# Kernel tuning notes

Hardware: AMD Instinct MI355X
Metric: run time of the kernel (lower is better)

## Reference

```python
import jax, jax.numpy as jnp
import numpy as np

N_HEAD = 16
TEMPERATURE = 1.0
LORA_SCALING = 16.0 / 8.0  # lora_alpha / r


def setup_inputs() -> dict:
    key = jax.random.key(0)
    B, S, D, E, R = 4, 1024, 1024, 8, 8
    ks = jax.random.split(key, 24)
    it = iter(ks)

    def nrm(shape, s):
        return (jax.random.normal(next(it), shape, jnp.float32) * s)

    inp = {}
    inp['x'] = jax.random.normal(next(it), (B, S, D), jnp.float32)
    inp['conv_w'] = nrm((D, D, 3), 0.02)
    inp['conv_b'] = jnp.zeros((D,), jnp.float32)
    inp['pool_w'] = nrm((1, D), 0.02)
    inp['pool_b'] = jnp.zeros((1,), jnp.float32)
    inp['rlin_w'] = nrm((E, D), 0.02)
    inp['rlin_b'] = jnp.zeros((E,), jnp.float32)
    for p, has_bias in (('q', True), ('k', False), ('v', True), ('o', True)):
        inp[p + 'W'] = nrm((D, D), 0.02)
        if has_bias:
            inp[p + 'b'] = jnp.zeros((D,), jnp.float32)
        inp[p + 'A'] = nrm((E, R, D), 0.02)
        inp[p + 'B'] = nrm((E, D, R), 0.02)
    return inp


def _router(x, conv_w, conv_b, pool_w, pool_b, rlin_w, rlin_b):
    # Conv1d(kernel=3, padding=1) over sequence, channels = n_state
    xc = jax.lax.conv_general_dilated(
        x.transpose(0, 2, 1), conv_w, (1,), [(1, 1)],
        dimension_numbers=('NCH', 'OIH', 'NCH')) + conv_b[None, :, None]
    xp = xc.transpose(0, 2, 1)                      # [B, S, D]
    scores = xp @ pool_w.T + pool_b                 # [B, S, 1]
    w = jax.nn.softmax(scores, axis=1)
    pooled = jnp.sum(w * xp, axis=1)                # [B, D]
    logits = pooled @ rlin_w.T + rlin_b             # [B, E]
    return jax.nn.softmax(logits / TEMPERATURE, axis=-1)


def _moe_linear(x, W, b, A, Bm, route):
    base = x @ W.T
    if b is not None:
        base = base + b
    h = jnp.einsum('bsd,erd->besr', x, A)           # [B, E, S, r]
    lora = jnp.einsum('besr,enr,be->bsn', h, Bm, route)
    return base + LORA_SCALING * lora


def reference(x, conv_w, conv_b, pool_w, pool_b, rlin_w, rlin_b,
              qW, qb, qA, qB, kW, kA, kB, vW, vb, vA, vB, oW, ob, oA, oB):
    B, S, D = x.shape
    H = N_HEAD
    dh = D // H
    route = _router(x, conv_w, conv_b, pool_w, pool_b, rlin_w, rlin_b)

    q = _moe_linear(x, qW, qb, qA, qB, route)
    k = _moe_linear(x, kW, None, kA, kB, route)
    v = _moe_linear(x, vW, vb, vA, vB, route)

    scale = dh ** (-0.25)
    qh = q.reshape(B, S, H, dh).transpose(0, 2, 1, 3) * scale   # [B,H,S,dh]
    kh = k.reshape(B, S, H, dh).transpose(0, 2, 3, 1) * scale   # [B,H,dh,S]
    vh = v.reshape(B, S, H, dh).transpose(0, 2, 1, 3)           # [B,H,S,dh]

    qk = (qh @ kh).astype(jnp.float32)                          # [B,H,S,S]
    w = jax.nn.softmax(qk, axis=-1).astype(q.dtype)
    wv = (w @ vh).transpose(0, 2, 1, 3).reshape(B, S, D)

    out = _moe_linear(wv, oW, ob, oA, oB, route)
    return out, qk
```

## Files before the change

kernel.cpp:

```cpp
#include <hip/hip_runtime.h>
#include <cstdint>

typedef unsigned short u16;
typedef __bf16 bf16_t;
typedef bf16_t bf16x8 __attribute__((ext_vector_type(8)));
typedef float f32x4 __attribute__((ext_vector_type(4)));

#define B_ 4
#define S_ 1024
#define D_ 1024
#define E_ 8
#define R_ 8
#define H_ 16
#define DH_ 64

#define GLOAD16(gp, lp) __builtin_amdgcn_global_load_lds( \
        (const __attribute__((address_space(1))) void*)(gp), \
        (__attribute__((address_space(3))) void*)(lp), 16, 0, 0)

static __device__ __forceinline__ u16 f2b(float f){
    union { float f; uint32_t i; } v; v.f = f;
    uint32_t i = v.i;
    uint32_t r = i + 0x7FFFu + ((i >> 16) & 1u);
    return (u16)(r >> 16);
}

__global__ void k_cvtall(const float4* x, const float* qB, const float* kB,
                         const float* vB, const float* oB,
                         ushort4* x16, ushort4* B16v, float4* cwp4){
    const int NX = B_*S_*D_/4;
    const int NB = E_*D_*R_/4;
    const int NC = 3*D_/4;
    const int NTOT = NX + 4*NB + NC;
    for (int i = blockIdx.x*blockDim.x + threadIdx.x; i < NTOT; i += gridDim.x*blockDim.x){
        if (i < NX){
            float4 v = x[i];
            ushort4 o; o.x=f2b(v.x); o.y=f2b(v.y); o.z=f2b(v.z); o.w=f2b(v.w);
            x16[i] = o;
        } else if (i < NX + 4*NB){
            int j = i - NX;
            int p = j >> 14, e = j & (NB-1);
            const float4* src = (p==0)?(const float4*)qB:(p==1)?(const float4*)kB
                              :(p==2)?(const float4*)vB:(const float4*)oB;
            float4 v = src[e];
            ushort4 o; o.x=f2b(v.x); o.y=f2b(v.y); o.z=f2b(v.z); o.w=f2b(v.w);
            B16v[p*NB + e] = o;
        } else {
            cwp4[i - NX - 4*NB] = make_float4(0.f,0.f,0.f,0.f);
        }
    }
}

__global__ void k_cwp(const float* conv_w, const float* conv_b, const float* pool_w,
                      const float* pool_b, float* cwp, float* constk){
    __shared__ float red[256];
    int bid = blockIdx.x, ob = blockIdx.y;
    if (bid < 12){
        int j = bid*256 + threadIdx.x;
        int t = j >> 10, i = j & 1023;
        float acc = 0.f;
        for (int o = ob*128; o < (ob+1)*128; ++o)
            acc += pool_w[o] * conv_w[(size_t)o*3072 + i*3 + t];
        atomicAdd(&cwp[j], acc);
    } else if (ob == 0){
        float acc = 0.f;
        for (int o = threadIdx.x; o < D_; o += 256) acc += pool_w[o] * conv_b[o];
        red[threadIdx.x] = acc; __syncthreads();
        for (int s = 128; s > 0; s >>= 1){
            if (threadIdx.x < s) red[threadIdx.x] += red[threadIdx.x+s];
            __syncthreads();
        }
        if (threadIdx.x == 0) *constk = red[0] + pool_b[0];
    }
}

__global__ void k_h(const float* x, const float* cwp, float* h){
    int b = blockIdx.y;
    int w = threadIdx.x >> 6, lane = threadIdx.x & 63;
    int s = blockIdx.x*4 + w;
    const float4* xr = (const float4*)(x + ((size_t)b*S_ + s)*D_);
    const float4* c0 = (const float4*)(cwp);
    const float4* c1 = (const float4*)(cwp + D_);
    const float4* c2 = (const float4*)(cwp + 2*D_);
    float a0 = 0.f, a1 = 0.f, a2 = 0.f;
    #pragma unroll
    for (int it = 0; it < 4; ++it){
        float4 v  = xr[it*64 + lane];
        float4 w0 = c0[it*64 + lane];
        float4 w1 = c1[it*64 + lane];
        float4 w2 = c2[it*64 + lane];
        a0 += v.x*w0.x + v.y*w0.y + v.z*w0.z + v.w*w0.w;
        a1 += v.x*w1.x + v.y*w1.y + v.z*w1.z + v.w*w1.w;
        a2 += v.x*w2.x + v.y*w2.y + v.z*w2.z + v.w*w2.w;
    }
    for (int off = 32; off; off >>= 1){
        a0 += __shfl_down(a0, off);
        a1 += __shfl_down(a1, off);
        a2 += __shfl_down(a2, off);
    }
    if (lane == 0){
        h[(0*B_ + b)*S_ + s] = a0;
        h[(1*B_ + b)*S_ + s] = a1;
        h[(2*B_ + b)*S_ + s] = a2;
    }
}

__global__ void k_xw(const float* x, const float* h, const float* constk, float* xwl){
    int b = blockIdx.y;
    int lane = threadIdx.x & 63;
    int w = threadIdx.x >> 6;
    int i = blockIdx.x*64 + lane;
    __shared__ float red[256];
    __shared__ float wsm_l[S_];
    __shared__ float red3[3][4][64];
    const float* h0 = h + (0*B_ + b)*S_;
    const float* h1 = h + (1*B_ + b)*S_;
    const float* h2 = h + (2*B_ + b)*S_;
    float ck = *constk;
    float mx = -1e30f;
    for (int s = threadIdx.x; s < S_; s += 256){
        float v = h1[s] + ck;
        if (s >= 1)   v += h0[s-1];
        if (s+1 < S_) v += h2[s+1];
        wsm_l[s] = v;
        mx = fmaxf(mx, v);
    }
    red[threadIdx.x] = mx; __syncthreads();
    for (int st = 128; st > 0; st >>= 1){
        if (threadIdx.x < st) red[threadIdx.x] = fmaxf(red[threadIdx.x], red[threadIdx.x+st]);
        __syncthreads();
    }
    mx = red[0]; __syncthreads();
    float sum = 0.f;
    for (int s = threadIdx.x; s < S_; s += 256) sum += __expf(wsm_l[s] - mx);
    red[threadIdx.x] = sum; __syncthreads();
    for (int st = 128; st > 0; st >>= 1){
        if (threadIdx.x < st) red[threadIdx.x] += red[threadIdx.x+st];
        __syncthreads();
    }
    float inv = 1.f / red[0];
    __syncthreads();
    for (int s = threadIdx.x; s < S_; s += 256)
        wsm_l[s] = __expf(wsm_l[s] - mx) * inv;
    __syncthreads();
    const float* xb = x + (size_t)b*S_*D_;
    float a0 = 0.f, a1 = 0.f, a2 = 0.f;
    #pragma unroll 4
    for (int r = w*256; r < (w+1)*256; ++r){
        float xv = xb[(size_t)r*D_ + i];
        float w1 = wsm_l[r];
        float w0 = (r+1 < S_) ? wsm_l[r+1] : 0.f;
        float w2 = (r >= 1)   ? wsm_l[r-1] : 0.f;
        a0 += w0*xv; a1 += w1*xv; a2 += w2*xv;
    }
    red3[0][w][lane] = a0; red3[1][w][lane] = a1; red3[2][w][lane] = a2;
    __syncthreads();
    if (w == 0){
        a0 = red3[0][0][lane] + red3[0][1][lane] + red3[0][2][lane] + red3[0][3][lane];
        a1 = red3[1][0][lane] + red3[1][1][lane] + red3[1][2][lane] + red3[1][3][lane];
        a2 = red3[2][0][lane] + red3[2][1][lane] + red3[2][2][lane] + red3[2][3][lane];
        xwl[b*3072 + i*3 + 0] = a0;
        xwl[b*3072 + i*3 + 1] = a1;
        xwl[b*3072 + i*3 + 2] = a2;
    }
}

__global__ void k_pooled(const float* conv_w, const float* conv_b, const float* xwl, float* pooled){
    int o = blockIdx.x*4 + (threadIdx.x >> 6);
    int lane = threadIdx.x & 63;
    const float* cw = conv_w + (size_t)o*3072;
    float a0=0.f, a1=0.f, a2=0.f, a3=0.f;
    for (int j = lane; j < 3072; j += 64){
        float c = cw[j];
        a0 += c*xwl[j]; a1 += c*xwl[3072+j]; a2 += c*xwl[2*3072+j]; a3 += c*xwl[3*3072+j];
    }
    for (int off = 32; off; off >>= 1){
        a0 += __shfl_down(a0, off); a1 += __shfl_down(a1, off);
        a2 += __shfl_down(a2, off); a3 += __shfl_down(a3, off);
    }
    if (lane == 0){
        float cb = conv_b[o];
        pooled[0*D_+o] = a0+cb; pooled[1*D_+o] = a1+cb;
        pooled[2*D_+o] = a2+cb; pooled[3*D_+o] = a3+cb;
    }
}

__global__ void k_route(const float* pooled, const float* rlin_w, const float* rlin_b, float* route){
    __shared__ float lg[B_][E_];
    int t = threadIdx.x;
    int b = t >> 6, e = (t >> 3) & 7, part = t & 7;
    float acc = 0.f;
    for (int o = part; o < D_; o += 8) acc += pooled[b*D_+o] * rlin_w[e*D_+o];
    acc += __shfl_down(acc, 4); acc += __shfl_down(acc, 2); acc += __shfl_down(acc, 1);
    if (part == 0) lg[b][e] = acc + rlin_b[e];
    __syncthreads();
    if (t < B_){
        float mx = -1e30f;
        for (int e2 = 0; e2 < E_; ++e2) mx = fmaxf(mx, lg[t][e2]);
        float ex[E_], sum = 0.f;
        for (int e2 = 0; e2 < E_; ++e2){ ex[e2] = expf(lg[t][e2]-mx); sum += ex[e2]; }
        for (int e2 = 0; e2 < E_; ++e2) route[t*E_+e2] = ex[e2]/sum;
    }
}

__global__ void k_aeff(const float* qA, const float* kA, const float* vA, const float* oA,
                       const float* route, u16* AeffT){
    int dc = blockIdx.x, b = blockIdx.y, p = blockIdx.z;
    const float* Ap = (p==0)?qA:(p==1)?kA:(p==2)?vA:oA;
    int z = p*4 + b;
    for (int idx = threadIdx.x; idx < 64*64; idx += 256){
        int dl = idx >> 6, kk = idx & 63;
        int d = dc*64 + dl;
        int e = kk >> 3, r = kk & 7;
        float v = 2.0f * route[b*E_+e] * Ap[(size_t)(e*R_+r)*D_ + d];
        AeffT[((size_t)z*D_ + d)*64 + kk] = f2b(v);
    }
}

__global__ __launch_bounds__(256) void k_weff(
        const u16* B16,
        const float* qW, const float* kW, const float* vW, const float* oW,
        const u16* AeffT, u16* Weff){
    __shared__ __align__(16) u16 As[128*64];
    __shared__ __align__(16) u16 Bs[128*64];
    int z = blockIdx.z, p = z >> 2;
    const u16* Bp = B16 + (size_t)p*E_*D_*R_;
    const float* Wp = (p==0)?qW:(p==1)?kW:(p==2)?vW:oW;
    int n0 = blockIdx.x*128, d0 = blockIdx.y*128;
    int tid = threadIdx.x;
    int e = tid & 7, row = tid >> 3;
    for (int pass = 0; pass < 4; ++pass){
        int rr = row + pass*32;
        GLOAD16(&Bp[((size_t)e*D_ + (n0+rr))*R_],           &As[pass*2048 + tid*8]);
        GLOAD16(&AeffT[((size_t)z*D_ + (d0+rr))*64 + e*8],  &Bs[pass*2048 + tid*8]);
    }
    __syncthreads();
    int l = tid & 63, w = tid >> 6;
    int wm = (w & 1)*64, wn = (w >> 1)*64;
    int lr = l & 15, quad = l >> 4;
    f32x4 acc[4][4] = {};
    for (int kk = 0; kk < 64; kk += 32){
        bf16x8 af[4], bg[4];
        for (int i = 0; i < 4; ++i) af[i] = *(const bf16x8*)&As[(wm + i*16 + lr)*64 + kk + quad*8];
        for (int j = 0; j < 4; ++j) bg[j] = *(const bf16x8*)&Bs[(wn + j*16 + lr)*64 + kk + quad*8];
        for (int i = 0; i < 4; ++i)
            for (int j = 0; j < 4; ++j)
                acc[i][j] = __builtin_amdgcn_mfma_f32_16x16x32_bf16(af[i], bg[j], acc[i][j], 0, 0, 0);
    }
    u16* Wz = Weff + (size_t)z*D_*D_;
    for (int i = 0; i < 4; ++i)
        for (int j = 0; j < 4; ++j)
            for (int r2 = 0; r2 < 4; ++r2){
                int n = n0 + wm + i*16 + quad*4 + r2;
                int d = d0 + wn + j*16 + lr;
                Wz[(size_t)n*D_ + d] = f2b(acc[i][j][r2] + Wp[(size_t)n*D_ + d]);
            }
}

static __device__ __forceinline__ void gemm_body(
        const u16* __restrict__ A, int lda,
        const u16* __restrict__ Bw,
        u16* Cb, float* Cf, int ldc,
        const float* bias, float scale, int K,
        int m0, int n0)
{
    __shared__ __align__(16) u16 As[128*32];
    __shared__ __align__(16) u16 Bs[128*32];
    int tid = threadIdx.x;
    int srow = tid >> 2, skc = (tid & 3)*8;
    u16* asd = &As[tid*8];
    u16* bsd = &Bs[tid*8];
    const u16* ga0 = &A [(size_t)(m0+srow)*lda + skc];
    const u16* ga1 = &A [(size_t)(m0+srow+64)*lda + skc];
    const u16* gb0 = &Bw[(size_t)(n0+srow)*D_ + skc];
    const u16* gb1 = &Bw[(size_t)(n0+srow+64)*D_ + skc];
    int l = tid & 63, w = tid >> 6;
    int wm = (w & 1)*64, wn = (w >> 1)*64;
    int lr = l & 15, quad = l >> 4;
    f32x4 acc[4][4] = {};
    for (int k0 = 0; k0 < K; k0 += 32){
        __syncthreads();
        GLOAD16(ga0 + k0, asd);
        GLOAD16(ga1 + k0, asd + 2048);
        GLOAD16(gb0 + k0, bsd);
        GLOAD16(gb1 + k0, bsd + 2048);
        __syncthreads();
        bf16x8 af[4], bg[4];
        for (int i = 0; i < 4; ++i) af[i] = *(const bf16x8*)&As[(wm + i*16 + lr)*32 + quad*8];
        for (int j = 0; j < 4; ++j) bg[j] = *(const bf16x8*)&Bs[(wn + j*16 + lr)*32 + quad*8];
        for (int i = 0; i < 4; ++i)
            for (int j = 0; j < 4; ++j)
                acc[i][j] = __builtin_amdgcn_mfma_f32_16x16x32_bf16(af[i], bg[j], acc[i][j], 0, 0, 0);
    }
    for (int j = 0; j < 4; ++j){
        int n = n0 + wn + j*16 + lr;
        float bv = bias ? bias[n] : 0.f;
        for (int i = 0; i < 4; ++i){
            int mrow = m0 + wm + i*16 + quad*4;
            for (int r2 = 0; r2 < 4; ++r2){
                float val = (acc[i][j][r2] + bv) * scale;
                size_t idx = (size_t)(mrow+r2)*ldc + n;
                if (Cf) __builtin_nontemporal_store(val, &Cf[idx]);
                else    Cb[idx] = f2b(val);
            }
        }
    }
}

__global__ __launch_bounds__(256) void k_gemm_qkv(
        const u16* x16, const u16* Weff, u16* qkv, const float* qb, const float* vb){
    int z = blockIdx.z, p = z >> 2, b = z & 3;
    const float* bias = (p==0) ? qb : (p==2) ? vb : (const float*)nullptr;
    float scale = (p==2) ? 1.0f : 0.35355339059327373f;
    gemm_body(x16 + (size_t)b*S_*D_, D_,
              Weff + (size_t)z*D_*D_,
              qkv + (size_t)z*S_*D_, (float*)nullptr, D_,
              bias, scale, 1024, blockIdx.x*128, blockIdx.y*128);
}

__global__ __launch_bounds__(256) void k_gemm_o(
        const u16* wv, const u16* WeffO, float* out, const float* ob){
    int b = blockIdx.z;
    gemm_body(wv + (size_t)b*S_*D_, D_,
              WeffO + (size_t)b*D_*D_,
              (u16*)nullptr, out + (size_t)b*S_*D_, D_,
              ob, 1.0f, 1024, blockIdx.x*128, blockIdx.y*128);
}

__global__ void k_vtrans(const u16* v, u16* vT){
    __shared__ __align__(16) u16 Tl[64*72];
    int st = blockIdx.x, bh = blockIdx.y;
    int b = bh >> 4, h = bh & 15;
    int tid = threadIdx.x;
    int row = tid >> 3, c = (tid & 7)*8;
    const u16* vb = v + (size_t)b*S_*D_ + h*64;
    for (int pass = 0; pass < 2; ++pass){
        int r = row + pass*32;
        *(uint4*)&Tl[r*72 + c] = *(const uint4*)&vb[(size_t)(st*64 + r)*D_ + c];
    }
    __syncthreads();
    u16* vTb = vT + (size_t)bh*64*S_;
    for (int pass = 0; pass < 2; ++pass){
        int dr = row + pass*32;
        union { u16 s[8]; uint4 u; } tmp;
        for (int j = 0; j < 8; ++j) tmp.s[j] = Tl[(c+j)*72 + dr];
        *(uint4*)&vTb[(size_t)dr*S_ + st*64 + c] = tmp.u;
    }
}

__global__ __launch_bounds__(256) void k_attn(const u16* q, const u16* k, const u16* vT,
                                              float* qk_out, u16* wv){
    __shared__ __align__(16) u16 Ql[64*64];
    __shared__ __align__(16) u16 Kl[64*64];
    __shared__ __align__(16) u16 Vt[64*64];
    __shared__ __align__(16) u16 Pl[64*64];
    int qt = blockIdx.x, bh = blockIdx.y;
    int b = bh >> 4, h = bh & 15;
    int q0 = qt*64;
    int tid = threadIdx.x;
    int l = tid & 63, w = tid >> 6;
    int lr = l & 15, quad = l >> 4;
    int srow = tid >> 3;
    int scol = (((tid & 7) ^ ((tid >> 3) & 7))) * 8;
    int sdst = tid * 8;
    const u16* qp  = q  + (size_t)b*S_*D_ + h*64;
    const u16* kp  = k  + (size_t)b*S_*D_ + h*64;
    const u16* vTp = vT + (size_t)bh*64*S_;
    float* qko = qk_out + (size_t)bh*S_*S_;
    GLOAD16(&qp[(size_t)(q0 + srow)*D_ + scol],      &Ql[sdst]);
    GLOAD16(&qp[(size_t)(q0 + srow + 32)*D_ + scol], &Ql[sdst + 2048]);
    int rsw = lr & 7;
    f32x4 oacc[4] = {};
    float m_i[4], l_i[4];
    for (int r2 = 0; r2 < 4; ++r2){ m_i[r2] = -1e30f; l_i[r2] = 0.f; }
    for (int t0 = 0; t0 < S_; t0 += 64){
        __syncthreads();
        GLOAD16(&kp[(size_t)(t0 + srow)*D_ + scol],        &Kl[sdst]);
        GLOAD16(&kp[(size_t)(t0 + srow + 32)*D_ + scol],   &Kl[sdst + 2048]);
        GLOAD16(&vTp[(size_t)srow*S_ + t0 + scol],         &Vt[sdst]);
        GLOAD16(&vTp[(size_t)(srow + 32)*S_ + t0 + scol],  &Vt[sdst + 2048]);
        __syncthreads();
        f32x4 sacc[4] = {};
        for (int kk = 0; kk < 64; kk += 32){
            int un = ((quad + (kk >> 3)) ^ rsw) * 8;
            bf16x8 aq = *(const bf16x8*)&Ql[(w*16 + lr)*64 + un];
            for (int jn = 0; jn < 4; ++jn){
                bf16x8 bk = *(const bf16x8*)&Kl[(jn*16 + lr)*64 + un];
                sacc[jn] = __builtin_amdgcn_mfma_f32_16x16x32_bf16(aq, bk, sacc[jn], 0, 0, 0);
            }
        }
        for (int jn = 0; jn < 4; ++jn)
            for (int r2 = 0; r2 < 4; ++r2){
                int sq = q0 + w*16 + quad*4 + r2;
                __builtin_nontemporal_store(sacc[jn][r2], &qko[(size_t)sq*S_ + t0 + jn*16 + lr]);
            }
        float alpha[4];
        for (int r2 = 0; r2 < 4; ++r2){
            float mx = fmaxf(fmaxf(sacc[0][r2], sacc[1][r2]), fmaxf(sacc[2][r2], sacc[3][r2]));
            for (int off = 1; off < 16; off <<= 1) mx = fmaxf(mx, __shfl_xor(mx, off));
            float mnew = fmaxf(m_i[r2], mx);
            alpha[r2] = __expf(m_i[r2] - mnew);
            m_i[r2] = mnew;
        }
        f32x4 p[4];
        for (int jn = 0; jn < 4; ++jn)
            for (int r2 = 0; r2 < 4; ++r2)
                p[jn][r2] = __expf(sacc[jn][r2] - m_i[r2]);
        for (int r2 = 0; r2 < 4; ++r2){
            float s = p[0][r2] + p[1][r2] + p[2][r2] + p[3][r2];
            for (int off = 1; off < 16; off <<= 1) s += __shfl_xor(s, off);
            l_i[r2] = l_i[r2]*alpha[r2] + s;
        }
        for (int jn = 0; jn < 4; ++jn)
            for (int r2 = 0; r2 < 4; ++r2)
                oacc[jn][r2] *= alpha[r2];
        for (int jn = 0; jn < 4; ++jn)
            for (int r2 = 0; r2 < 4; ++r2){
                int pr = w*16 + quad*4 + r2;
                int tu = (jn*2 + (lr >> 3)) ^ (pr & 7);
                Pl[pr*64 + tu*8 + (lr & 7)] = f2b(p[jn][r2]);
            }
        for (int kk = 0; kk < 64; kk += 32){
            int un = ((quad + (kk >> 3)) ^ rsw) * 8;
            bf16x8 ap = *(const bf16x8*)&Pl[(w*16 + lr)*64 + un];
            for (int jn = 0; jn < 4; ++jn){
                bf16x8 bv = *(const bf16x8*)&Vt[(jn*16 + lr)*64 + un];
                oacc[jn] = __builtin_amdgcn_mfma_f32_16x16x32_bf16(ap, bv, oacc[jn], 0, 0, 0);
            }
        }
    }
    u16* wvp = wv + (size_t)b*S_*D_ + h*64;
    for (int r2 = 0; r2 < 4; ++r2){
        float inv = 1.f / l_i[r2];
        int sq = q0 + w*16 + quad*4 + r2;
        for (int jn = 0; jn < 4; ++jn)
            wvp[(size_t)sq*D_ + jn*16 + lr] = f2b(oacc[jn][r2] * inv);
    }
}

extern "C" void kernel_launch(void* const* d_in, const int* in_sizes, int n_in,
                              void* d_out, int out_size, void* d_ws, size_t ws_size,
                              hipStream_t stream){
    const float* x      = (const float*)d_in[0];
    const float* conv_w = (const float*)d_in[1];
    const float* conv_b = (const float*)d_in[2];
    const float* pool_w = (const float*)d_in[3];
    const float* pool_b = (const float*)d_in[4];
    const float* rlin_w = (const float*)d_in[5];
    const float* rlin_b = (const float*)d_in[6];
    const float* qW = (const float*)d_in[7];
    const float* qb = (const float*)d_in[8];
    const float* qA = (const float*)d_in[9];
    const float* qB = (const float*)d_in[10];
    const float* kW = (const float*)d_in[11];
    const float* kA = (const float*)d_in[12];
    const float* kB = (const float*)d_in[13];
    const float* vW = (const float*)d_in[14];
    const float* vb = (const float*)d_in[15];
    const float* vA = (const float*)d_in[16];
    const float* vB = (const float*)d_in[17];
    const float* oW = (const float*)d_in[18];
    const float* ob = (const float*)d_in[19];
    const float* oA = (const float*)d_in[20];
    const float* oB = (const float*)d_in[21];

    char* ws = (char*)d_ws;
    float* route  = (float*)(ws + 0);
    float* constk = (float*)(ws + 512);
    float* cwp    = (float*)(ws + 1024);
    float* h      = (float*)(ws + 16384);
    float* xwl    = (float*)(ws + 81920);
    float* pooled = (float*)(ws + 131072);
    u16* AeffT = (u16*)(ws + (1ull  << 20));
    u16* B16   = (u16*)(ws + (3ull  << 20));
    u16* Weff  = (u16*)(ws + (4ull  << 20));
    u16* x16   = (u16*)(ws + (36ull << 20));
    u16* qkv   = (u16*)(ws + (44ull << 20));
    u16* qbuf  = qkv + 0*(size_t)B_*S_*D_;
    u16* kbuf  = qkv + 1*(size_t)B_*S_*D_;
    u16* vbuf  = qkv + 2*(size_t)B_*S_*D_;
    u16* vTbuf = (u16*)(ws + (68ull << 20));
    u16* wvbuf = vbuf;

    float* out    = (float*)d_out;
    float* qk_out = out + (size_t)B_*S_*D_;

    const long long sDD = (long long)D_*D_;

    k_cvtall<<<2048, 256, 0, stream>>>((const float4*)x, qB, kB, vB, oB,
                                       (ushort4*)x16, (ushort4*)B16, (float4*)cwp);

    k_cwp   <<<dim3(13, 8), 256, 0, stream>>>(conv_w, conv_b, pool_w, pool_b, cwp, constk);
    k_h     <<<dim3(S_/4, B_), 256, 0, stream>>>(x, cwp, h);
    k_xw    <<<dim3(16, B_), 256, 0, stream>>>(x, h, constk, xwl);
    k_pooled<<<256, 256, 0, stream>>>(conv_w, conv_b, xwl, pooled);
    k_route <<<1, 256, 0, stream>>>(pooled, rlin_w, rlin_b, route);
    k_aeff  <<<dim3(16, B_, 4), 256, 0, stream>>>(qA, kA, vA, oA, route, AeffT);
    k_weff  <<<dim3(8, 8, 16), 256, 0, stream>>>(B16, qW, kW, vW, oW, AeffT, Weff);

    k_gemm_qkv<<<dim3(8,8,12), 256, 0, stream>>>(x16, Weff, qkv, qb, vb);

    k_vtrans<<<dim3(16, B_*H_), 256, 0, stream>>>(vbuf, vTbuf);
    k_attn  <<<dim3(16, B_*H_), 256, 0, stream>>>(qbuf, kbuf, vTbuf, qk_out, wvbuf);
    k_gemm_o<<<dim3(8,8,B_), 256, 0, stream>>>(wvbuf, Weff + 12*sDD, out, ob);
}
```

Baseline: 615.1 us.

## Fuse prep kernels, route into aeff, V transpose into QKV GEMM, retile O GEMM

Merges the bf16 conversion and the conv-pool weight reduction into one launch. The reduction now writes partial sums that k_h adds up, which removes the zero-fill and the atomics. Router softmax is recomputed inside each k_aeff block, and the V transpose is done in the QKV GEMM epilogue through shared memory, so the k_route and k_vtrans launches and the V round trip go away. The output GEMM uses 128x64 tiles, doubling the grid. Costs are redundant routing work per block and extra syncs and shared memory in the QKV epilogue.

```diff
diff --git a/kernel.cpp b/kernel.cpp
--- a/kernel.cpp
+++ b/kernel.cpp
@@ -25,63 +25,70 @@
     return (u16)(r >> 16);
 }
 
-__global__ void k_cvtall(const float4* x, const float* qB, const float* kB,
-                         const float* vB, const float* oB,
-                         ushort4* x16, ushort4* B16v, float4* cwp4){
+__global__ void k_pre(const float4* x, const float* qB, const float* kB,
+                      const float* vB, const float* oB,
+                      const float* conv_w, const float* conv_b,
+                      const float* pool_w, const float* pool_b,
+                      ushort4* x16, ushort4* B16v, float* cwp_part, float* constk){
+    const int NCVT = 2048;
     const int NX = B_*S_*D_/4;
     const int NB = E_*D_*R_/4;
-    const int NC = 3*D_/4;
-    const int NTOT = NX + 4*NB + NC;
-    for (int i = blockIdx.x*blockDim.x + threadIdx.x; i < NTOT; i += gridDim.x*blockDim.x){
-        if (i < NX){
-            float4 v = x[i];
-            ushort4 o; o.x=f2b(v.x); o.y=f2b(v.y); o.z=f2b(v.z); o.w=f2b(v.w);
-            x16[i] = o;
-        } else if (i < NX + 4*NB){
-            int j = i - NX;
-            int p = j >> 14, e = j & (NB-1);
-            const float4* src = (p==0)?(const float4*)qB:(p==1)?(const float4*)kB
-                              :(p==2)?(const float4*)vB:(const float4*)oB;
-            float4 v = src[e];
-            ushort4 o; o.x=f2b(v.x); o.y=f2b(v.y); o.z=f2b(v.z); o.w=f2b(v.w);
-            B16v[p*NB + e] = o;
+    if (blockIdx.x < NCVT){
+        const int NTOT = NX + 4*NB;
+        for (int i = blockIdx.x*blockDim.x + threadIdx.x; i < NTOT; i += NCVT*blockDim.x){
+            if (i < NX){
+                float4 v = x[i];
+                ushort4 o; o.x=f2b(v.x); o.y=f2b(v.y); o.z=f2b(v.z); o.w=f2b(v.w);
+                x16[i] = o;
+            } else {
+                int j = i - NX;
+                int p = j >> 14, e = j & (NB-1);
+                const float4* src = (p==0)?(const float4*)qB:(p==1)?(const float4*)kB
+                                  :(p==2)?(const float4*)vB:(const float4*)oB;
+                float4 v = src[e];
+                ushort4 o; o.x=f2b(v.x); o.y=f2b(v.y); o.z=f2b(v.z); o.w=f2b(v.w);
+                B16v[p*NB + e] = o;
+            }
+        }
+    } else {
+        int idx = blockIdx.x - NCVT;
+        if (idx < 96){
+            int bid = idx % 12, ob = idx / 12;
+            int j = bid*256 + threadIdx.x;
+            int t = j >> 10, i = j & 1023;
+            float acc = 0.f;
+            for (int o = ob*128; o < ob*128 + 128; ++o)
+                acc += pool_w[o] * conv_w[(size_t)o*3072 + i*3 + t];
+            cwp_part[ob*3072 + j] = acc;
         } else {
-            cwp4[i - NX - 4*NB] = make_float4(0.f,0.f,0.f,0.f);
-        }
-    }
-}
-
-__global__ void k_cwp(const float* conv_w, const float* conv_b, const float* pool_w,
-                      const float* pool_b, float* cwp, float* constk){
-    __shared__ float red[256];
-    int bid = blockIdx.x, ob = blockIdx.y;
-    if (bid < 12){
-        int j = bid*256 + threadIdx.x;
-        int t = j >> 10, i = j & 1023;
-        float acc = 0.f;
-        for (int o = ob*128; o < (ob+1)*128; ++o)
-            acc += pool_w[o] * conv_w[(size_t)o*3072 + i*3 + t];
-        atomicAdd(&cwp[j], acc);
-    } else if (ob == 0){
-        float acc = 0.f;
-        for (int o = threadIdx.x; o < D_; o += 256) acc += pool_w[o] * conv_b[o];
-        red[threadIdx.x] = acc; __syncthreads();
-        for (int s = 128; s > 0; s >>= 1){
-            if (threadIdx.x < s) red[threadIdx.x] += red[threadIdx.x+s];
-            __syncthreads();
-        }
-        if (threadIdx.x == 0) *constk = red[0] + pool_b[0];
-    }
-}
-
-__global__ void k_h(const float* x, const float* cwp, float* h){
+            __shared__ float red[256];
+            float acc = 0.f;
+            for (int o = threadIdx.x; o < D_; o += 256) acc += pool_w[o] * conv_b[o];
+            red[threadIdx.x] = acc; __syncthreads();
+            for (int s = 128; s > 0; s >>= 1){
+                if (threadIdx.x < s) red[threadIdx.x] += red[threadIdx.x+s];
+                __syncthreads();
+            }
+            if (threadIdx.x == 0) *constk = red[0] + pool_b[0];
+        }
+    }
+}
+
+__global__ void k_h(const float* x, const float* cwp_part, float* h){
+    __shared__ float cw[3072];
     int b = blockIdx.y;
+    for (int j = threadIdx.x; j < 3072; j += 256){
+        float s = 0.f;
+        for (int ob = 0; ob < 8; ++ob) s += cwp_part[ob*3072 + j];
+        cw[j] = s;
+    }
+    __syncthreads();
     int w = threadIdx.x >> 6, lane = threadIdx.x & 63;
     int s = blockIdx.x*4 + w;
     const float4* xr = (const float4*)(x + ((size_t)b*S_ + s)*D_);
-    const float4* c0 = (const float4*)(cwp);
-    const float4* c1 = (const float4*)(cwp + D_);
-    const float4* c2 = (const float4*)(cwp + 2*D_);
+    const float4* c0 = (const float4*)(cw);
+    const float4* c1 = (const float4*)(cw + D_);
+    const float4* c2 = (const float4*)(cw + 2*D_);
     float a0 = 0.f, a1 = 0.f, a2 = 0.f;
     #pragma unroll
     for (int it = 0; it < 4; ++it){
@@ -185,34 +192,34 @@
     }
 }
 
-__global__ void k_route(const float* pooled, const float* rlin_w, const float* rlin_b, float* route){
-    __shared__ float lg[B_][E_];
-    int t = threadIdx.x;
-    int b = t >> 6, e = (t >> 3) & 7, part = t & 7;
-    float acc = 0.f;
-    for (int o = part; o < D_; o += 8) acc += pooled[b*D_+o] * rlin_w[e*D_+o];
-    acc += __shfl_down(acc, 4); acc += __shfl_down(acc, 2); acc += __shfl_down(acc, 1);
-    if (part == 0) lg[b][e] = acc + rlin_b[e];
-    __syncthreads();
-    if (t < B_){
-        float mx = -1e30f;
-        for (int e2 = 0; e2 < E_; ++e2) mx = fmaxf(mx, lg[t][e2]);
-        float ex[E_], sum = 0.f;
-        for (int e2 = 0; e2 < E_; ++e2){ ex[e2] = expf(lg[t][e2]-mx); sum += ex[e2]; }
-        for (int e2 = 0; e2 < E_; ++e2) route[t*E_+e2] = ex[e2]/sum;
-    }
-}
-
 __global__ void k_aeff(const float* qA, const float* kA, const float* vA, const float* oA,
-                       const float* route, u16* AeffT){
+                       const float* pooled, const float* rlin_w, const float* rlin_b,
+                       u16* AeffT){
+    __shared__ float rt[E_];
     int dc = blockIdx.x, b = blockIdx.y, p = blockIdx.z;
+    {
+        int e = threadIdx.x >> 5, part = threadIdx.x & 31;
+        float acc = 0.f;
+        for (int o = part; o < D_; o += 32) acc += pooled[b*D_+o] * rlin_w[e*D_+o];
+        for (int off = 16; off; off >>= 1) acc += __shfl_xor(acc, off);
+        if (part == 0) rt[e] = acc + rlin_b[e];
+        __syncthreads();
+        if (threadIdx.x == 0){
+            float mx = -1e30f;
+            for (int e2 = 0; e2 < E_; ++e2) mx = fmaxf(mx, rt[e2]);
+            float ex[E_], sum = 0.f;
+            for (int e2 = 0; e2 < E_; ++e2){ ex[e2] = expf(rt[e2]-mx); sum += ex[e2]; }
+            for (int e2 = 0; e2 < E_; ++e2) rt[e2] = ex[e2]/sum;
+        }
+        __syncthreads();
+    }
     const float* Ap = (p==0)?qA:(p==1)?kA:(p==2)?vA:oA;
     int z = p*4 + b;
     for (int idx = threadIdx.x; idx < 64*64; idx += 256){
         int dl = idx >> 6, kk = idx & 63;
         int d = dc*64 + dl;
         int e = kk >> 3, r = kk & 7;
-        float v = 2.0f * route[b*E_+e] * Ap[(size_t)(e*R_+r)*D_ + d];
+        float v = 2.0f * rt[e] * Ap[(size_t)(e*R_+r)*D_ + d];
         AeffT[((size_t)z*D_ + d)*64 + kk] = f2b(v);
     }
 }
@@ -257,28 +264,28 @@
             }
 }
 
-static __device__ __forceinline__ void gemm_body(
-        const u16* __restrict__ A, int lda,
-        const u16* __restrict__ Bw,
-        u16* Cb, float* Cf, int ldc,
-        const float* bias, float scale, int K,
-        int m0, int n0)
-{
+__global__ __launch_bounds__(256) void k_gemm_qkv(
+        const u16* x16, const u16* Weff, u16* qkv, u16* vT, const float* qb, const float* vb){
     __shared__ __align__(16) u16 As[128*32];
     __shared__ __align__(16) u16 Bs[128*32];
+    __shared__ __align__(16) u16 T[64*72];
+    int z = blockIdx.z, p = z >> 2, b = z & 3;
+    const u16* A  = x16 + (size_t)b*S_*D_;
+    const u16* Bw = Weff + (size_t)z*D_*D_;
+    int m0 = blockIdx.x*128, n0 = blockIdx.y*128;
     int tid = threadIdx.x;
     int srow = tid >> 2, skc = (tid & 3)*8;
     u16* asd = &As[tid*8];
     u16* bsd = &Bs[tid*8];
-    const u16* ga0 = &A [(size_t)(m0+srow)*lda + skc];
-    const u16* ga1 = &A [(size_t)(m0+srow+64)*lda + skc];
+    const u16* ga0 = &A [(size_t)(m0+srow)*D_ + skc];
+    const u16* ga1 = &A [(size_t)(m0+srow+64)*D_ + skc];
     const u16* gb0 = &Bw[(size_t)(n0+srow)*D_ + skc];
     const u16* gb1 = &Bw[(size_t)(n0+srow+64)*D_ + skc];
     int l = tid & 63, w = tid >> 6;
     int wm = (w & 1)*64, wn = (w >> 1)*64;
     int lr = l & 15, quad = l >> 4;
     f32x4 acc[4][4] = {};
-    for (int k0 = 0; k0 < K; k0 += 32){
+    for (int k0 = 0; k0 < D_; k0 += 32){
         __syncthreads();
         GLOAD16(ga0 + k0, asd);
         GLOAD16(ga1 + k0, asd + 2048);
@@ -292,59 +299,89 @@
             for (int j = 0; j < 4; ++j)
                 acc[i][j] = __builtin_amdgcn_mfma_f32_16x16x32_bf16(af[i], bg[j], acc[i][j], 0, 0, 0);
     }
-    for (int j = 0; j < 4; ++j){
+    if (p < 2){
+        const float* bias = (p==0) ? qb : (const float*)nullptr;
+        const float scale = 0.35355339059327373f;
+        u16* Cb = qkv + (size_t)z*S_*D_;
+        for (int j = 0; j < 4; ++j){
+            int n = n0 + wn + j*16 + lr;
+            float bv = bias ? bias[n] : 0.f;
+            for (int i = 0; i < 4; ++i){
+                int mrow = m0 + wm + i*16 + quad*4;
+                for (int r2 = 0; r2 < 4; ++r2)
+                    Cb[(size_t)(mrow+r2)*D_ + n] = f2b((acc[i][j][r2] + bv)*scale);
+            }
+        }
+    } else {
+        for (int c = 0; c < 4; ++c){
+            if (w == c){
+                for (int j = 0; j < 4; ++j){
+                    int col = j*16 + lr;
+                    float bv = vb[n0 + (c>>1)*64 + col];
+                    for (int i = 0; i < 4; ++i)
+                        for (int r2 = 0; r2 < 4; ++r2){
+                            int row = i*16 + quad*4 + r2;
+                            T[row*72 + col] = f2b(acc[i][j][r2] + bv);
+                        }
+                }
+            }
+            __syncthreads();
+            int bh = b*16 + (n0 >> 6) + (c >> 1);
+            int s0 = m0 + (c & 1)*64;
+            int dh = tid >> 2, sp = (tid & 3)*16;
+            union { u16 u[8]; uint4 q; } t0_, t1_;
+            for (int jj = 0; jj < 8; ++jj){
+                t0_.u[jj] = T[(sp+jj)*72 + dh];
+                t1_.u[jj] = T[(sp+8+jj)*72 + dh];
+            }
+            *(uint4*)&vT[((size_t)bh*64 + dh)*S_ + s0 + sp]     = t0_.q;
+            *(uint4*)&vT[((size_t)bh*64 + dh)*S_ + s0 + sp + 8] = t1_.q;
+            __syncthreads();
+        }
+    }
+}
+
+__global__ __launch_bounds__(256) void k_gemm_o(
+        const u16* wv, const u16* WeffO, float* out, const float* ob_){
+    __shared__ __align__(16) u16 As[128*32];
+    __shared__ __align__(16) u16 Bs[64*32];
+    int b = blockIdx.z;
+    const u16* A  = wv + (size_t)b*S_*D_;
+    const u16* Bw = WeffO + (size_t)b*D_*D_;
+    float* Cf = out + (size_t)b*S_*D_;
+    int m0 = blockIdx.x*128, n0 = blockIdx.y*64;
+    int tid = threadIdx.x;
+    int srow = tid >> 2, skc = (tid & 3)*8;
+    u16* asd = &As[tid*8];
+    u16* bsd = &Bs[tid*8];
+    const u16* ga0 = &A [(size_t)(m0+srow)*D_ + skc];
+    const u16* ga1 = &A [(size_t)(m0+srow+64)*D_ + skc];
+    const u16* gb0 = &Bw[(size_t)(n0+srow)*D_ + skc];
+    int l = tid & 63, w = tid >> 6;
+    int wm = (w & 1)*64, wn = (w >> 1)*32;
+    int lr = l & 15, quad = l >> 4;
+    f32x4 acc[4][2] = {};
+    for (int k0 = 0; k0 < D_; k0 += 32){
+        __syncthreads();
+        GLOAD16(ga0 + k0, asd);
+        GLOAD16(ga1 + k0, asd + 2048);
+        GLOAD16(gb0 + k0, bsd);
+        __syncthreads();
+        bf16x8 af[4], bg[2];
+        for (int i = 0; i < 4; ++i) af[i] = *(const bf16x8*)&As[(wm + i*16 + lr)*32 + quad*8];
+        for (int j = 0; j < 2; ++j) bg[j] = *(const bf16x8*)&Bs[(wn + j*16 + lr)*32 + quad*8];
+        for (int i = 0; i < 4; ++i)
+            for (int j = 0; j < 2; ++j)
+                acc[i][j] = __builtin_amdgcn_mfma_f32_16x16x32_bf16(af[i], bg[j], acc[i][j], 0, 0, 0);
+    }
+    for (int j = 0; j < 2; ++j){
         int n = n0 + wn + j*16 + lr;
-        float bv = bias ? bias[n] : 0.f;
+        float bv = ob_[n];
         for (int i = 0; i < 4; ++i){
             int mrow = m0 + wm + i*16 + quad*4;
-            for (int r2 = 0; r2 < 4; ++r2){
-                float val = (acc[i][j][r2] + bv) * scale;
-                size_t idx = (size_t)(mrow+r2)*ldc + n;
-                if (Cf) __builtin_nontemporal_store(val, &Cf[idx]);
-                else    Cb[idx] = f2b(val);
-            }
-        }
-    }
-}
-
-__global__ __launch_bounds__(256) void k_gemm_qkv(
-        const u16* x16, const u16* Weff, u16* qkv, const float* qb, const float* vb){
-    int z = blockIdx.z, p = z >> 2, b = z & 3;
-    const float* bias = (p==0) ? qb : (p==2) ? vb : (const float*)nullptr;
-    float scale = (p==2) ? 1.0f : 0.35355339059327373f;
-    gemm_body(x16 + (size_t)b*S_*D_, D_,
-              Weff + (size_t)z*D_*D_,
-              qkv + (size_t)z*S_*D_, (float*)nullptr, D_,
-              bias, scale, 1024, blockIdx.x*128, blockIdx.y*128);
-}
-
-__global__ __launch_bounds__(256) void k_gemm_o(
-        const u16* wv, const u16* WeffO, float* out, const float* ob){
-    int b = blockIdx.z;
-    gemm_body(wv + (size_t)b*S_*D_, D_,
-              WeffO + (size_t)b*D_*D_,
-              (u16*)nullptr, out + (size_t)b*S_*D_, D_,
-              ob, 1.0f, 1024, blockIdx.x*128, blockIdx.y*128);
-}
-
-__global__ void k_vtrans(const u16* v, u16* vT){
-    __shared__ __align__(16) u16 Tl[64*72];
-    int st = blockIdx.x, bh = blockIdx.y;
-    int b = bh >> 4, h = bh & 15;
-    int tid = threadIdx.x;
-    int row = tid >> 3, c = (tid & 7)*8;
-    const u16* vb = v + (size_t)b*S_*D_ + h*64;
-    for (int pass = 0; pass < 2; ++pass){
-        int r = row + pass*32;
-        *(uint4*)&Tl[r*72 + c] = *(const uint4*)&vb[(size_t)(st*64 + r)*D_ + c];
-    }
-    __syncthreads();
-    u16* vTb = vT + (size_t)bh*64*S_;
-    for (int pass = 0; pass < 2; ++pass){
-        int dr = row + pass*32;
-        union { u16 s[8]; uint4 u; } tmp;
-        for (int j = 0; j < 8; ++j) tmp.s[j] = Tl[(c+j)*72 + dr];
-        *(uint4*)&vTb[(size_t)dr*S_ + st*64 + c] = tmp.u;
+            for (int r2 = 0; r2 < 4; ++r2)
+                __builtin_nontemporal_store(acc[i][j][r2] + bv, &Cf[(size_t)(mrow+r2)*D_ + n]);
+        }
     }
 }
 
@@ -465,12 +502,11 @@
     const float* oB = (const float*)d_in[21];
 
     char* ws = (char*)d_ws;
-    float* route  = (float*)(ws + 0);
-    float* constk = (float*)(ws + 512);
-    float* cwp    = (float*)(ws + 1024);
-    float* h      = (float*)(ws + 16384);
-    float* xwl    = (float*)(ws + 81920);
-    float* pooled = (float*)(ws + 131072);
+    float* constk   = (float*)(ws + 512);
+    float* cwp_part = (float*)(ws + 1024);
+    float* h        = (float*)(ws + 131072);
+    float* xwl      = (float*)(ws + 196608);
+    float* pooled   = (float*)(ws + 262144);
     u16* AeffT = (u16*)(ws + (1ull  << 20));
     u16* B16   = (u16*)(ws + (3ull  << 20));
     u16* Weff  = (u16*)(ws + (4ull  << 20));
@@ -487,20 +523,15 @@
 
     const long long sDD = (long long)D_*D_;
 
-    k_cvtall<<<2048, 256, 0, stream>>>((const float4*)x, qB, kB, vB, oB,
-                                       (ushort4*)x16, (ushort4*)B16, (float4*)cwp);
-
-    k_cwp   <<<dim3(13, 8), 256, 0, stream>>>(conv_w, conv_b, pool_w, pool_b, cwp, constk);
-    k_h     <<<dim3(S_/4, B_), 256, 0, stream>>>(x, cwp, h);
+    k_pre<<<2145, 256, 0, stream>>>((const float4*)x, qB, kB, vB, oB,
+                                    conv_w, conv_b, pool_w, pool_b,
+                                    (ushort4*)x16, (ushort4*)B16, cwp_part, constk);
+    k_h     <<<dim3(S_/4, B_), 256, 0, stream>>>(x, cwp_part, h);
     k_xw    <<<dim3(16, B_), 256, 0, stream>>>(x, h, constk, xwl);
     k_pooled<<<256, 256, 0, stream>>>(conv_w, conv_b, xwl, pooled);
-    k_route <<<1, 256, 0, stream>>>(pooled, rlin_w, rlin_b, route);
-    k_aeff  <<<dim3(16, B_, 4), 256, 0, stream>>>(qA, kA, vA, oA, route, AeffT);
+    k_aeff  <<<dim3(16, B_, 4), 256, 0, stream>>>(qA, kA, vA, oA, pooled, rlin_w, rlin_b, AeffT);
     k_weff  <<<dim3(8, 8, 16), 256, 0, stream>>>(B16, qW, kW, vW, oW, AeffT, Weff);
-
-    k_gemm_qkv<<<dim3(8,8,12), 256, 0, stream>>>(x16, Weff, qkv, qb, vb);
-
-    k_vtrans<<<dim3(16, B_*H_), 256, 0, stream>>>(vbuf, vTbuf);
+    k_gemm_qkv<<<dim3(8,8,12), 256, 0, stream>>>(x16, Weff, qkv, vTbuf, qb, vb);
     k_attn  <<<dim3(16, B_*H_), 256, 0, stream>>>(qbuf, kbuf, vTbuf, qk_out, wvbuf);
-    k_gemm_o<<<dim3(8,8,B_), 256, 0, stream>>>(wvbuf, Weff + 12*sDD, out, ob);
-}
+    k_gemm_o<<<dim3(8,16,B_), 256, 0, stream>>>(wvbuf, Weff + 12*sDD, out, ob);
+}
```

After: 580.0 us (median of 2 runs). 5.7% less time.
